# Optimization experiments

Measured on AMD Instinct MI355X. Metric: run time of the kernel, lower is better.

The kernel has to match this reference:

```python
import jax, jax.numpy as jnp
import numpy as np

W_CE = 0.1
W_BOUND = 0.1
SMOOTH = 1e-06
IGNORE_INDEX = -100


def _edt_to_seeds(seed):
    """Exact Euclidean distance to nearest True pixel (Felzenszwalb-style separable EDT).

    seed: [H, W] bool. Returns [H, W] float32 distances (0 at seed pixels).
    Equivalent to scipy.ndimage.distance_transform_edt(~seed ... ) semantics:
    distance from every pixel to the nearest seed pixel.
    """
    H, W = seed.shape
    BIG = jnp.float32(H + W)  # upper bound on any in-image distance
    x = jnp.arange(W, dtype=jnp.float32)
    # 1D horizontal distance to nearest seed in the same row
    pos_l = jnp.where(seed, x, jnp.float32(-1e9))
    left = jax.lax.cummax(pos_l, axis=1)
    dl = x - left
    pos_r = jnp.where(seed, x, jnp.float32(1e9))
    right = jax.lax.cummin(pos_r, axis=1, reverse=True)
    dr = right - x
    d1 = jnp.minimum(jnp.minimum(dl, dr), BIG)  # [H, W], capped to avoid overflow
    g2 = d1 * d1  # squared horizontal distances
    # Vertical lower-envelope pass: dist2[y,x] = min_y' (y-y')^2 + g2[y',x]
    y = jnp.arange(H, dtype=jnp.float32)
    diff2 = (y[:, None] - y[None, :]) ** 2  # [H, H]
    dist2 = jnp.min(diff2[:, :, None] + g2[None, :, :], axis=1)  # [H, W]
    return jnp.sqrt(dist2)


def _signed_distance(class_mask):
    """signed = EDT(~mask) - EDT(mask) per scipy convention; 0 if mask empty."""
    has_pos = class_mask.any()
    has_neg = jnp.logical_not(class_mask).any()
    dist_out = _edt_to_seeds(class_mask)            # dist to nearest inside pixel (0 inside)
    dist_in = _edt_to_seeds(jnp.logical_not(class_mask))  # dist to nearest outside pixel (0 outside)
    signed = jnp.where(has_neg, dist_out - dist_in, dist_out)
    return jnp.where(has_pos, signed, jnp.zeros_like(signed))


def _dist_maps(targets, valid, num_classes):
    B, H, W = targets.shape
    t_safe = jnp.where(valid, targets, 0)
    cls = jnp.arange(num_classes, dtype=t_safe.dtype)
    cm = (t_safe[:, None, :, :] == cls[None, :, None, None]) & valid[:, None, :, :]  # [B,C,H,W]
    flat = cm.reshape(B * num_classes, H, W)
    signed = jax.lax.map(_signed_distance, flat).reshape(B, num_classes, H, W)
    return signed * valid[:, None, :, :].astype(jnp.float32)  # zero out invalid pixels


def setup_inputs() -> dict:
    key = jax.random.key(0)
    k1, k2 = jax.random.split(key)
    inputs = jax.random.normal(k1, (4, 8, 256, 256), dtype=jnp.float32)
    targets = jax.random.randint(k2, (4, 256, 256), 0, 8, dtype=jnp.int32)
    return {"inputs": inputs, "targets": targets}


def reference(inputs, targets):
    B, C, H, W = inputs.shape
    logp = jax.nn.log_softmax(inputs, axis=1)
    probs = jnp.exp(logp)
    # CrossEntropyLoss (all targets valid, mean over B*H*W)
    ce = -jnp.mean(jnp.take_along_axis(logp, targets[:, None, :, :].astype(jnp.int32), axis=1))
    # Dice loss (valid mask = targets >= 0)
    valid_d = targets >= 0
    t_safe = jnp.where(valid_d, targets, 0)
    onehot = jax.nn.one_hot(t_safe, C, dtype=jnp.float32).transpose(0, 3, 1, 2)  # [B,C,H,W]
    vm = valid_d[:, None, :, :].astype(jnp.float32)
    ps = probs * vm
    th = onehot * vm
    intersection = jnp.sum(ps * th)
    cardinality = jnp.sum(ps + th)
    dice = 1.0 - (2.0 * intersection + SMOOTH) / (cardinality + SMOOTH)
    dice_total = W_CE * ce + (1.0 - W_CE) * dice  # DiceCELoss.forward
    # Boundary loss (signed distance maps, mean reduction)
    valid_b = (targets != IGNORE_INDEX) & (targets >= 0) & (targets < C)
    dmaps = _dist_maps(targets, valid_b, C)
    vbf = valid_b[:, None, :, :].astype(jnp.float32)
    bound = jnp.sum(probs * dmaps * vbf) / (jnp.sum(vbf) + 1e-08)
    return W_CE * ce + (1.0 - W_CE - W_BOUND) * dice_total + W_BOUND * bound
```

## Files before the change

kernel.cpp:

```cpp
#include <hip/hip_runtime.h>
#include <math.h>

#define B_DIM 4
#define C_DIM 8
#define H_DIM 256
#define W_DIM 256
#define HW 65536
#define NPIX 262144


__device__ __forceinline__ float wave_reduce_f(float v) {
#pragma unroll
    for (int off = 32; off; off >>= 1) v += __shfl_xor(v, off, 64);
    return v;
}

__global__ void __launch_bounds__(256) k_row(
    const float* __restrict__ x, const int* __restrict__ tgt,
    float* __restrict__ lse_out, float* __restrict__ pce, float* __restrict__ pinter,
    int2* __restrict__ pcnt, unsigned long long* __restrict__ wmask_g,
    float* __restrict__ bound_part, unsigned int* __restrict__ cnt,
    unsigned int* __restrict__ gdone) {
    int bi = blockIdx.x;
    int b = bi >> 8, y = bi & 255;
    int i = threadIdx.x;
    int lane = i & 63, wid = i >> 6;
    size_t rowbase = (size_t)b * HW + (size_t)y * W_DIM;

    if (bi == 0) {
        if (i < 32) { bound_part[i << 5] = 0.0f; cnt[i << 5] = 0u; }
        if (i == 32) *gdone = 0u;
    }

    const float* xb = x + (size_t)b * C_DIM * HW + (size_t)y * W_DIM + i;
    float v[C_DIM];
    float m = -1e30f;
#pragma unroll
    for (int c = 0; c < C_DIM; ++c) { v[c] = xb[(size_t)c * HW]; m = fmaxf(m, v[c]); }
    float s = 0.f;
#pragma unroll
    for (int c = 0; c < C_DIM; ++c) s += __expf(v[c] - m);
    float lse = m + __logf(s);
    lse_out[rowbase + i] = lse;

    int t = tgt[rowbase + i];
    bool valid_d = (t >= 0);
    bool valid_b = valid_d && (t < C_DIM);
    int tc = valid_b ? t : 0;
    float vt = v[0];
#pragma unroll
    for (int c = 1; c < C_DIM; ++c) vt = (tc == c) ? v[c] : vt;

    float ce = lse - vt;
    float inter = valid_b ? __expf(vt - lse) : 0.f;

    __shared__ float ws_ce[4], ws_in[4];
    __shared__ int ws_cd[4], ws_cb[4];
    float r_ce = wave_reduce_f(ce);
    float r_in = wave_reduce_f(inter);
    unsigned long long md = __ballot(valid_d);
    unsigned long long mbv = __ballot(valid_b);
    if (lane == 0) {
        ws_ce[wid] = r_ce; ws_in[wid] = r_in;
        ws_cd[wid] = __popcll(md); ws_cb[wid] = __popcll(mbv);
    }

    __shared__ unsigned long long wmask[C_DIM][4];
#pragma unroll
    for (int c = 0; c < C_DIM; ++c) {
        unsigned long long mc = __ballot(valid_b && (t == c));
        if (lane == 0) wmask[c][wid] = mc;
    }
    __syncthreads();

    if (i == 0) {
        pce[bi] = (ws_ce[0] + ws_ce[1]) + (ws_ce[2] + ws_ce[3]);
        pinter[bi] = (ws_in[0] + ws_in[1]) + (ws_in[2] + ws_in[3]);
        pcnt[bi] = make_int2((ws_cd[0] + ws_cd[1]) + (ws_cd[2] + ws_cd[3]),
                             (ws_cb[0] + ws_cb[1]) + (ws_cb[2] + ws_cb[3]));
    }
    if (i < 32) {
        int c = i >> 2, w = i & 3;
        wmask_g[((size_t)((b * C_DIM + c) * 256 + y) << 2) + w] = wmask[c][w];
    }
}

#define LDS_PITCH 18
#define ENVELOPE(H, MA, MB)                                                     \
    {                                                                           \
        float4 qa0 = *(const float4*)&H[ybase][tx << 2];                        \
        float4 qb0 = *(const float4*)&H[ybase + 1][tx << 2];                    \
        MA.x = fminf(qa0.x, qb0.x + 1.0f); MB.x = fminf(qb0.x, qa0.x + 1.0f);   \
        MA.y = fminf(qa0.y, qb0.y + 1.0f); MB.y = fminf(qb0.y, qa0.y + 1.0f);   \
        MA.z = fminf(qa0.z, qb0.z + 1.0f); MB.z = fminf(qb0.z, qa0.z + 1.0f);   \
        MA.w = fminf(qa0.w, qb0.w + 1.0f); MB.w = fminf(qb0.w, qa0.w + 1.0f);   \
        int s = 1;                                                              \
        for (;;) {                                                              \
            int ra = max(ybase - s, 0);                                         \
            int rb = min(ybase + 1 + s, H_DIM - 1);                             \
            float4 qa = *(const float4*)&H[ra][tx << 2];                        \
            float4 qb = *(const float4*)&H[rb][tx << 2];                        \
            float s2a = (float)(s * s);                                         \
            float s2b = (float)((s + 1) * (s + 1));                             \
            MA.x = fminf(MA.x, fminf(qa.x + s2a, qb.x + s2b));                  \
            MA.y = fminf(MA.y, fminf(qa.y + s2a, qb.y + s2b));                  \
            MA.z = fminf(MA.z, fminf(qa.z + s2a, qb.z + s2b));                  \
            MA.w = fminf(MA.w, fminf(qa.w + s2a, qb.w + s2b));                  \
            MB.x = fminf(MB.x, fminf(qa.x + s2b, qb.x + s2a));                  \
            MB.y = fminf(MB.y, fminf(qa.y + s2b, qb.y + s2a));                  \
            MB.z = fminf(MB.z, fminf(qa.z + s2b, qb.z + s2a));                  \
            MB.w = fminf(MB.w, fminf(qa.w + s2b, qb.w + s2a));                  \
            float lmax = fmaxf(fmaxf(fmaxf(MA.x, MA.y), fmaxf(MA.z, MA.w)),     \
                               fmaxf(fmaxf(MB.x, MB.y), fmaxf(MB.z, MB.w)));    \
            ++s;                                                                \
            float st = (float)(s * s);                                          \
            if (s >= H_DIM || __all(st >= lmax)) break;                         \
        }                                                                       \
    }

__global__ void __launch_bounds__(512) k_cols(
    const unsigned long long* __restrict__ wmask_g, const float* __restrict__ x,
    const float* __restrict__ lse, const int* __restrict__ tgt,
    const float* __restrict__ pce, const float* __restrict__ pinter,
    const int2* __restrict__ pcnt,
    float* __restrict__ bound_part, unsigned int* __restrict__ cnt,
    unsigned int* __restrict__ gdone, float* __restrict__ out) {
    int blk = blockIdx.x;
    int bc = blk >> 4;
    int xt = blk & 15;
    int b = bc >> 3, c = bc & 7;
    int tid = threadIdx.x;
    int tx = tid & 3;
    int ybase = (tid >> 2) << 1;
    int lane = tid & 63, wid = tid >> 6;

    __shared__ float h0s[H_DIM][LDS_PITCH];
    __shared__ float h1s[H_DIM][LDS_PITCH];
    __shared__ int anyf[2];
    __shared__ float wsum[8];
    __shared__ int sh_last;
    double* dred = (double*)&h0s[0][0];

    size_t pixbase = (size_t)b * HW;
    size_t xplane = ((size_t)b * C_DIM + c) * HW;
    int x0 = (xt << 4) + (tx << 2);
    size_t row0 = (size_t)ybase * W_DIM + x0;
    size_t row1 = row0 + W_DIM;
    float4 xv0 = *(const float4*)(x + xplane + row0);
    float4 xv1 = *(const float4*)(x + xplane + row1);
    float4 lv0 = *(const float4*)(lse + pixbase + row0);
    float4 lv1 = *(const float4*)(lse + pixbase + row1);
    int4 tv0 = *(const int4*)(tgt + pixbase + row0);
    int4 tv1 = *(const int4*)(tgt + pixbase + row1);

    int srow = tid & 255;
    int pol = tid >> 8;
    const unsigned long long* mrow = wmask_g + ((size_t)(bc * 256 + srow) << 2);
    unsigned long long w0 = mrow[0], w1 = mrow[1], w2 = mrow[2], w3 = mrow[3];

    if (tid < 2) anyf[tid] = 0;
    __syncthreads();
    if (pol == 0) {
        unsigned long long orv = w0 | w1 | w2 | w3;
        unsigned long long bp = __ballot(orv != 0ull);
        if (lane == 0 && bp) atomicOr(&anyf[0], 1);
    } else {
        unsigned long long andv = w0 & w1 & w2 & w3;
        unsigned long long bn = __ballot(andv != ~0ull);
        if (lane == 0 && bn) atomicOr(&anyf[1], 1);
    }

    {
        unsigned long long q0 = pol ? ~w0 : w0;
        unsigned long long q1 = pol ? ~w1 : w1;
        unsigned long long q2 = pol ? ~w2 : w2;
        unsigned long long q3 = pol ? ~w3 : w3;
        int wi = xt >> 2;
        int b0base = (xt & 3) << 4;
        int gc0 = xt << 4;
        int wbase = wi << 6;
        int h0p = q0 ? (63 - __builtin_clzll(q0)) : -100000;
        int h1p = q1 ? (127 - __builtin_clzll(q1)) : h0p;
        int h2p = q2 ? (191 - __builtin_clzll(q2)) : h1p;
        int lastp = (wi == 0) ? -100000 : (wi == 1) ? h0p : (wi == 2) ? h1p : h2p;
        int l3p = q3 ? (192 + __builtin_ctzll(q3)) : 100000;
        int l2p = q2 ? (128 + __builtin_ctzll(q2)) : l3p;
        int l1p = q1 ? (64 + __builtin_ctzll(q1)) : l2p;
        int nextp = (wi == 0) ? l1p : (wi == 1) ? l2p : (wi == 2) ? l3p : 100000;
        unsigned long long wn = (wi == 0) ? q0 : (wi == 1) ? q1 : (wi == 2) ? q2 : q3;
        unsigned long long lowmask = (b0base == 0) ? 0ull : ((~0ull) >> (64 - b0base));
        unsigned long long wlow = wn & lowmask;
        int lastw = wlow ? (wbase + 63 - __builtin_clzll(wlow)) : lastp;
        int hib = b0base + 16;
        unsigned long long whigh = (hib == 64) ? 0ull : (wn & ((~0ull) << hib));
        int nextw = whigh ? (wbase + __builtin_ctzll(whigh)) : nextp;
        unsigned int wseg = (unsigned int)((wn >> b0base) & 0xFFFFull);

        int d1l[16], d1r[16];
        int dl = gc0 - lastw;
#pragma unroll
        for (int i2 = 0; i2 < 16; ++i2) {
            dl = ((wseg >> i2) & 1u) ? 0 : dl;
            d1l[i2] = dl;
            ++dl;
        }
        int dr = nextw - (gc0 + 15);
#pragma unroll
        for (int i2 = 15; i2 >= 0; --i2) {
            dr = ((wseg >> i2) & 1u) ? 0 : dr;
            d1r[i2] = dr;
            ++dr;
        }
        float fd[16];
#pragma unroll
        for (int i2 = 0; i2 < 16; ++i2) {
            int d1 = min(min(d1l[i2], d1r[i2]), 512);
            fd[i2] = (float)d1 * (float)d1;
        }
        float (*hp)[LDS_PITCH] = pol ? h1s : h0s;
        *(float4*)&hp[srow][0]  = make_float4(fd[0], fd[1], fd[2], fd[3]);
        *(float4*)&hp[srow][4]  = make_float4(fd[4], fd[5], fd[6], fd[7]);
        *(float4*)&hp[srow][8]  = make_float4(fd[8], fd[9], fd[10], fd[11]);
        *(float4*)&hp[srow][12] = make_float4(fd[12], fd[13], fd[14], fd[15]);
    }
    __syncthreads();

    float4 m0a, m0b, m1a, m1b;
    ENVELOPE(h0s, m0a, m0b)
    ENVELOPE(h1s, m1a, m1b)

    bool has_pos = anyf[0] != 0;
    bool has_neg = anyf[1] != 0;

    float lsum = 0.f;
#pragma unroll
    for (int iy = 0; iy < 2; ++iy) {
        float4 M0 = iy ? m0b : m0a;
        float4 M1 = iy ? m1b : m1a;
        float4 xv = iy ? xv1 : xv0;
        float4 lv = iy ? lv1 : lv0;
        int4 tv = iy ? tv1 : tv0;
#pragma unroll
        for (int j = 0; j < 4; ++j) {
            float d2o = (j == 0) ? M0.x : (j == 1) ? M0.y : (j == 2) ? M0.z : M0.w;
            float d2i = (j == 0) ? M1.x : (j == 1) ? M1.y : (j == 2) ? M1.z : M1.w;
            float dout = sqrtf(d2o), din = sqrtf(d2i);
            float sgn = has_pos ? (has_neg ? (dout - din) : dout) : 0.f;
            float xs = (j == 0) ? xv.x : (j == 1) ? xv.y : (j == 2) ? xv.z : xv.w;
            float ls = (j == 0) ? lv.x : (j == 1) ? lv.y : (j == 2) ? lv.z : lv.w;
            int tt   = (j == 0) ? tv.x : (j == 1) ? tv.y : (j == 2) ? tv.z : tv.w;
            bool vb = (tt >= 0) && (tt < C_DIM);
            float prob = __expf(xs - ls);
            lsum += vb ? prob * sgn : 0.f;
        }
    }

    float r2 = wave_reduce_f(lsum);
    if (lane == 0) wsum[wid] = r2;
    __syncthreads();
    if (tid == 0) {
        float bsum = ((wsum[0] + wsum[1]) + (wsum[2] + wsum[3]))
                   + ((wsum[4] + wsum[5]) + (wsum[6] + wsum[7]));
        float old = atomicAdd(&bound_part[bc << 5], bsum);
        asm volatile("" :: "v"(old));
        unsigned int o = atomicAdd(&cnt[bc << 5], 1u);
        int lastflag = 0;
        if (o == 15u) {
            unsigned int g = atomicAdd(gdone, 1u);
            lastflag = (g == 31u) ? 1 : 0;
        }
        sh_last = lastflag;
    }
    __syncthreads();
    if (!sh_last) return;

    double s_ce = 0, s_in = 0, c_d = 0, c_b = 0;
    for (int k = tid; k < 1024; k += 512) {
        s_ce += (double)pce[k]; s_in += (double)pinter[k];
        int2 cc = pcnt[k]; c_d += (double)cc.x; c_b += (double)cc.y;
    }
    double sums[3]; double vin[3] = {s_ce, s_in, c_d * 4194304.0 + c_b};
    for (int q = 0; q < 3; ++q) {
        dred[tid] = vin[q];
        __syncthreads();
        for (int s2 = 256; s2; s2 >>= 1) { if (tid < s2) dred[tid] += dred[tid + s2]; __syncthreads(); }
        sums[q] = dred[0];
        __syncthreads();
    }
    __shared__ float bpart_s[32];
    if (tid < 32) bpart_s[tid] = atomicAdd(&bound_part[tid << 5], 0.0f);
    __syncthreads();
    if (tid == 0) {
        double btot = 0.0;
        for (int k = 0; k < 32; ++k) btot += (double)bpart_s[k];
        double packed = sums[2];
        double cd = floor(packed / 4194304.0 + 1e-9);
        double cb = packed - cd * 4194304.0;
        double ce = sums[0] / (double)NPIX;
        double inter = sums[1];
        double card = cd + cb;
        double dice = 1.0 - (2.0 * inter + 1e-6) / (card + 1e-6);
        double dice_total = 0.1 * ce + 0.9 * dice;
        double bound = btot / (cb + 1e-8);
        out[0] = (float)(0.1 * ce + 0.8 * dice_total + 0.1 * bound);
    }
}

extern "C" void kernel_launch(void* const* d_in, const int* in_sizes, int n_in,
                              void* d_out, int out_size, void* d_ws, size_t ws_size,
                              hipStream_t stream) {
    const float* x = (const float*)d_in[0];
    const int* tgt = (const int*)d_in[1];
    float* out = (float*)d_out;

    char* ws = (char*)d_ws;
    float* pce    = (float*)(ws + 0);
    float* pinter = (float*)(ws + 4096);
    int2*  pcnt   = (int2*)(ws + 8192);
    float* bound_part = (float*)(ws + 16384);
    unsigned int* cnt = (unsigned int*)(ws + 20480);
    unsigned int* gdone = (unsigned int*)(ws + 24576);
    float* lse    = (float*)(ws + 65536);
    unsigned long long* wmask_g = (unsigned long long*)(ws + (size_t)(2u << 20));

    k_row<<<1024, 256, 0, stream>>>(x, tgt, lse, pce, pinter, pcnt, wmask_g,
                                    bound_part, cnt, gdone);
    k_cols<<<512, 512, 0, stream>>>(wmask_g, x, lse, tgt, pce, pinter, pcnt,
                                    bound_part, cnt, gdone, out);
}
```

Before: 23.94 us.

## Split column EDT blocks into two row halves, one output row per thread

k_cols now launches twice as many blocks. Each block covers half the rows of a 16-column strip, and each thread computes the vertical lower envelope for a single row instead of a row pair. The goal is more parallelism and a shorter per-thread serial envelope loop with fewer live registers. In exchange, every block still recomputes the full 256-row horizontal distance pass into LDS, so that setup work is duplicated. The LDS pitch changes to 20 and the completion counter threshold moves to 32.

```diff
diff --git a/kernel.cpp b/kernel.cpp
--- a/kernel.cpp
+++ b/kernel.cpp
@@ -85,34 +85,33 @@
     }
 }
 
-#define LDS_PITCH 18
-#define ENVELOPE(H, MA, MB)                                                     \
+#define LDS_PITCH 20
+#define ENVELOPE1(H, MA)                                                        \
     {                                                                           \
-        float4 qa0 = *(const float4*)&H[ybase][tx << 2];                        \
-        float4 qb0 = *(const float4*)&H[ybase + 1][tx << 2];                    \
-        MA.x = fminf(qa0.x, qb0.x + 1.0f); MB.x = fminf(qb0.x, qa0.x + 1.0f);   \
-        MA.y = fminf(qa0.y, qb0.y + 1.0f); MB.y = fminf(qb0.y, qa0.y + 1.0f);   \
-        MA.z = fminf(qa0.z, qb0.z + 1.0f); MB.z = fminf(qb0.z, qa0.z + 1.0f);   \
-        MA.w = fminf(qa0.w, qb0.w + 1.0f); MB.w = fminf(qb0.w, qa0.w + 1.0f);   \
+        int col = tx << 2;                                                      \
+        MA = *(const float4*)&H[y][col];                                        \
         int s = 1;                                                              \
         for (;;) {                                                              \
-            int ra = max(ybase - s, 0);                                         \
-            int rb = min(ybase + 1 + s, H_DIM - 1);                             \
-            float4 qa = *(const float4*)&H[ra][tx << 2];                        \
-            float4 qb = *(const float4*)&H[rb][tx << 2];                        \
-            float s2a = (float)(s * s);                                         \
-            float s2b = (float)((s + 1) * (s + 1));                             \
-            MA.x = fminf(MA.x, fminf(qa.x + s2a, qb.x + s2b));                  \
-            MA.y = fminf(MA.y, fminf(qa.y + s2a, qb.y + s2b));                  \
-            MA.z = fminf(MA.z, fminf(qa.z + s2a, qb.z + s2b));                  \
-            MA.w = fminf(MA.w, fminf(qa.w + s2a, qb.w + s2b));                  \
-            MB.x = fminf(MB.x, fminf(qa.x + s2b, qb.x + s2a));                  \
-            MB.y = fminf(MB.y, fminf(qa.y + s2b, qb.y + s2a));                  \
-            MB.z = fminf(MB.z, fminf(qa.z + s2b, qb.z + s2a));                  \
-            MB.w = fminf(MB.w, fminf(qa.w + s2b, qb.w + s2a));                  \
-            float lmax = fmaxf(fmaxf(fmaxf(MA.x, MA.y), fmaxf(MA.z, MA.w)),     \
-                               fmaxf(fmaxf(MB.x, MB.y), fmaxf(MB.z, MB.w)));    \
-            ++s;                                                                \
+            int ra1 = max(y - s, 0);                                            \
+            int rb1 = min(y + s, H_DIM - 1);                                    \
+            int ra2 = max(y - s - 1, 0);                                        \
+            int rb2 = min(y + s + 1, H_DIM - 1);                                \
+            float4 qa1 = *(const float4*)&H[ra1][col];                          \
+            float4 qb1 = *(const float4*)&H[rb1][col];                          \
+            float4 qa2 = *(const float4*)&H[ra2][col];                          \
+            float4 qb2 = *(const float4*)&H[rb2][col];                          \
+            float s2_1 = (float)(s * s);                                        \
+            float s2_2 = (float)((s + 1) * (s + 1));                            \
+            MA.x = fminf(MA.x, fminf(fminf(qa1.x + s2_1, qb1.x + s2_1),         \
+                                     fminf(qa2.x + s2_2, qb2.x + s2_2)));       \
+            MA.y = fminf(MA.y, fminf(fminf(qa1.y + s2_1, qb1.y + s2_1),         \
+                                     fminf(qa2.y + s2_2, qb2.y + s2_2)));       \
+            MA.z = fminf(MA.z, fminf(fminf(qa1.z + s2_1, qb1.z + s2_1),         \
+                                     fminf(qa2.z + s2_2, qb2.z + s2_2)));       \
+            MA.w = fminf(MA.w, fminf(fminf(qa1.w + s2_1, qb1.w + s2_1),         \
+                                     fminf(qa2.w + s2_2, qb2.w + s2_2)));       \
+            float lmax = fmaxf(fmaxf(MA.x, MA.y), fmaxf(MA.z, MA.w));           \
+            s += 2;                                                             \
             float st = (float)(s * s);                                          \
             if (s >= H_DIM || __all(st >= lmax)) break;                         \
         }                                                                       \
@@ -126,12 +125,14 @@
     float* __restrict__ bound_part, unsigned int* __restrict__ cnt,
     unsigned int* __restrict__ gdone, float* __restrict__ out) {
     int blk = blockIdx.x;
-    int bc = blk >> 4;
-    int xt = blk & 15;
+    int bc = blk >> 5;
+    int sub = blk & 31;
+    int xt = sub >> 1;
+    int yh = sub & 1;
     int b = bc >> 3, c = bc & 7;
     int tid = threadIdx.x;
     int tx = tid & 3;
-    int ybase = (tid >> 2) << 1;
+    int y = (yh << 7) + (tid >> 2);
     int lane = tid & 63, wid = tid >> 6;
 
     __shared__ float h0s[H_DIM][LDS_PITCH];
@@ -139,19 +140,16 @@
     __shared__ int anyf[2];
     __shared__ float wsum[8];
     __shared__ int sh_last;
+    __shared__ float bpart_s[32];
     double* dred = (double*)&h0s[0][0];
 
     size_t pixbase = (size_t)b * HW;
     size_t xplane = ((size_t)b * C_DIM + c) * HW;
     int x0 = (xt << 4) + (tx << 2);
-    size_t row0 = (size_t)ybase * W_DIM + x0;
-    size_t row1 = row0 + W_DIM;
+    size_t row0 = (size_t)y * W_DIM + x0;
     float4 xv0 = *(const float4*)(x + xplane + row0);
-    float4 xv1 = *(const float4*)(x + xplane + row1);
     float4 lv0 = *(const float4*)(lse + pixbase + row0);
-    float4 lv1 = *(const float4*)(lse + pixbase + row1);
     int4 tv0 = *(const int4*)(tgt + pixbase + row0);
-    int4 tv1 = *(const int4*)(tgt + pixbase + row1);
 
     int srow = tid & 255;
     int pol = tid >> 8;
@@ -225,34 +223,26 @@
     }
     __syncthreads();
 
-    float4 m0a, m0b, m1a, m1b;
-    ENVELOPE(h0s, m0a, m0b)
-    ENVELOPE(h1s, m1a, m1b)
+    float4 m0a, m1a;
+    ENVELOPE1(h0s, m0a)
+    ENVELOPE1(h1s, m1a)
 
     bool has_pos = anyf[0] != 0;
     bool has_neg = anyf[1] != 0;
 
     float lsum = 0.f;
 #pragma unroll
-    for (int iy = 0; iy < 2; ++iy) {
-        float4 M0 = iy ? m0b : m0a;
-        float4 M1 = iy ? m1b : m1a;
-        float4 xv = iy ? xv1 : xv0;
-        float4 lv = iy ? lv1 : lv0;
-        int4 tv = iy ? tv1 : tv0;
-#pragma unroll
-        for (int j = 0; j < 4; ++j) {
-            float d2o = (j == 0) ? M0.x : (j == 1) ? M0.y : (j == 2) ? M0.z : M0.w;
-            float d2i = (j == 0) ? M1.x : (j == 1) ? M1.y : (j == 2) ? M1.z : M1.w;
-            float dout = sqrtf(d2o), din = sqrtf(d2i);
-            float sgn = has_pos ? (has_neg ? (dout - din) : dout) : 0.f;
-            float xs = (j == 0) ? xv.x : (j == 1) ? xv.y : (j == 2) ? xv.z : xv.w;
-            float ls = (j == 0) ? lv.x : (j == 1) ? lv.y : (j == 2) ? lv.z : lv.w;
-            int tt   = (j == 0) ? tv.x : (j == 1) ? tv.y : (j == 2) ? tv.z : tv.w;
-            bool vb = (tt >= 0) && (tt < C_DIM);
-            float prob = __expf(xs - ls);
-            lsum += vb ? prob * sgn : 0.f;
-        }
+    for (int j = 0; j < 4; ++j) {
+        float d2o = (j == 0) ? m0a.x : (j == 1) ? m0a.y : (j == 2) ? m0a.z : m0a.w;
+        float d2i = (j == 0) ? m1a.x : (j == 1) ? m1a.y : (j == 2) ? m1a.z : m1a.w;
+        float dout = sqrtf(d2o), din = sqrtf(d2i);
+        float sgn = has_pos ? (has_neg ? (dout - din) : dout) : 0.f;
+        float xs = (j == 0) ? xv0.x : (j == 1) ? xv0.y : (j == 2) ? xv0.z : xv0.w;
+        float ls = (j == 0) ? lv0.x : (j == 1) ? lv0.y : (j == 2) ? lv0.z : lv0.w;
+        int tt   = (j == 0) ? tv0.x : (j == 1) ? tv0.y : (j == 2) ? tv0.z : tv0.w;
+        bool vb = (tt >= 0) && (tt < C_DIM);
+        float prob = __expf(xs - ls);
+        lsum += vb ? prob * sgn : 0.f;
     }
 
     float r2 = wave_reduce_f(lsum);
@@ -265,7 +255,7 @@
         asm volatile("" :: "v"(old));
         unsigned int o = atomicAdd(&cnt[bc << 5], 1u);
         int lastflag = 0;
-        if (o == 15u) {
+        if (o == 31u) {
             unsigned int g = atomicAdd(gdone, 1u);
             lastflag = (g == 31u) ? 1 : 0;
         }
@@ -287,7 +277,6 @@
         sums[q] = dred[0];
         __syncthreads();
     }
-    __shared__ float bpart_s[32];
     if (tid < 32) bpart_s[tid] = atomicAdd(&bound_part[tid << 5], 0.0f);
     __syncthreads();
     if (tid == 0) {
@@ -325,6 +314,6 @@
 
     k_row<<<1024, 256, 0, stream>>>(x, tgt, lse, pce, pinter, pcnt, wmask_g,
                                     bound_part, cnt, gdone);
-    k_cols<<<512, 512, 0, stream>>>(wmask_g, x, lse, tgt, pce, pinter, pcnt,
-                                    bound_part, cnt, gdone, out);
+    k_cols<<<1024, 512, 0, stream>>>(wmask_g, x, lse, tgt, pce, pinter, pcnt,
+                                     bound_part, cnt, gdone, out);
 }
```

Measured after the change: 24.53 us. +2.5%, slower.
